# Kernel optimization log

Hardware: AMD Instinct MI355X
Metric: run time of the kernel (lower is better)

The kernel has to match this reference:

```python
import jax, jax.numpy as jnp
import numpy as np

HEADS = 16
HIDDEN = 1024
HEAD_DIM = HIDDEN // HEADS
NUM_RELATIONS = 100


def setup_inputs() -> dict:
    key = jax.random.key(0)
    ks = jax.random.split(key, 8)
    B, N, C = 4, 1024, HIDDEN
    x = jax.random.normal(ks[0], (B, N, C), dtype=jnp.float32)
    relations_mask = jax.random.randint(ks[1], (B, N, N), 0, NUM_RELATIONS, dtype=jnp.int64)
    s = 1.0 / np.sqrt(C)
    qkv_w = jax.random.uniform(ks[2], (3 * C, C), jnp.float32, -s, s)
    qkv_b = jax.random.uniform(ks[3], (3 * C,), jnp.float32, -s, s)
    proj_w = jax.random.uniform(ks[4], (C, C), jnp.float32, -s, s)
    proj_b = jax.random.uniform(ks[5], (C,), jnp.float32, -s, s)
    rel_emb = jax.random.normal(ks[6], (NUM_RELATIONS, HEAD_DIM), dtype=jnp.float32)
    return {"x": x, "relations_mask": relations_mask, "qkv_w": qkv_w,
            "qkv_b": qkv_b, "proj_w": proj_w, "proj_b": proj_b, "rel_emb": rel_emb}


def reference(x, relations_mask, qkv_w, qkv_b, proj_w, proj_b, rel_emb):
    B, N, C = x.shape
    H, d = HEADS, HEAD_DIM
    scale = d ** (-0.5)
    qkv = x @ qkv_w.T + qkv_b                       # [B, N, 3C]
    q, k, v = jnp.split(qkv, 3, axis=-1)
    to_heads = lambda t: t.reshape(B, N, H, d).transpose(0, 2, 1, 3)  # b h n d
    q, k, v = to_heads(q), to_heads(k), to_heads(v)
    dots = jnp.einsum('bhid,bhjd->bhij', q, k) * scale
    # einsum('bhij,bijd->bhijd', dots, bias).mean(-1) == dots * bias.mean(-1)
    rel_means = rel_emb.mean(-1)                    # [100]
    bias = rel_means[relations_mask]                # [B, N, N]
    dots = dots + dots * bias[:, None]              # broadcast over heads
    m = relations_mask.astype(dots.dtype)[:, None]  # hierarchy levels
    attn = jax.nn.softmax(dots * m + (1.0 - m) * (-1e9), axis=-1)
    out = jnp.einsum('bhij,bhjd->bhid', attn, v)
    out = out.transpose(0, 2, 1, 3).reshape(B, N, C)
    return out @ proj_w.T + proj_b
```

## Files before the change

### kernel.cpp

```cpp
#include <hip/hip_runtime.h>
#include <hip/hip_bf16.h>
#include <stdint.h>

constexpr int Bsz  = 4;
constexpr int Nseq = 1024;
constexpr int Cdim = 1024;
constexpr int Mrows = Bsz * Nseq;
constexpr int KD = 1024;
constexpr int BK = 64;
constexpr int NT = KD / BK;

typedef __attribute__((ext_vector_type(8))) short s16x8;
typedef __attribute__((ext_vector_type(4))) float f32x4;
typedef __attribute__((address_space(3))) unsigned char lds_b;
typedef __attribute__((address_space(1))) const unsigned char gbl_b;

__device__ inline short bf16_rne(float f) {
    union { float f; unsigned u; } c; c.f = f;
    unsigned u = c.u;
    u = u + 0x7FFFu + ((u >> 16) & 1u);
    return (short)(u >> 16);
}
__device__ inline float bf2f(unsigned short u) {
    union { unsigned u; float f; } c; c.u = ((unsigned)u) << 16;
    return c.f;
}

template <int N> __device__ __forceinline__ void waitv() {
    if constexpr (N == 0)      asm volatile("s_waitcnt vmcnt(0)" ::: "memory");
    else if constexpr (N == 4) asm volatile("s_waitcnt vmcnt(4)" ::: "memory");
    else if constexpr (N == 6) asm volatile("s_waitcnt vmcnt(6)" ::: "memory");
    else static_assert(N == 0, "unsupported vmcnt");
}

__global__ __launch_bounds__(256) void prep_kernel(const float* __restrict__ x,
                                                   const float* __restrict__ Wv,
                                                   const float* __restrict__ pw,
                                                   const float* __restrict__ bv,
                                                   const float* __restrict__ pb,
                                                   ushort* __restrict__ xb,
                                                   ushort* __restrict__ wvT,
                                                   ushort* __restrict__ pwb,
                                                   float* __restrict__ bias2) {
    const int bid = blockIdx.x;
    const int tid = threadIdx.x;
    if (bid < 256) {
        __shared__ ushort t[64][72];
        const int r0 = (bid >> 4) * 64, c0 = (bid & 15) * 64;
        const int lr = tid >> 4;
        const int lc = (tid & 15) * 4;
        #pragma unroll
        for (int p = 0; p < 4; ++p) {
            const int row = p * 16 + lr;
            const float4 v = *(const float4*)(Wv + (size_t)(r0 + row) * Cdim + c0 + lc);
            t[lc + 0][row] = (ushort)bf16_rne(v.x);
            t[lc + 1][row] = (ushort)bf16_rne(v.y);
            t[lc + 2][row] = (ushort)bf16_rne(v.z);
            t[lc + 3][row] = (ushort)bf16_rne(v.w);
        }
        __syncthreads();
        const int orow = tid >> 2;
        const int oc   = (tid & 3) * 16;
        const s16x8 a = *(const s16x8*)&t[orow][oc];
        const s16x8 b = *(const s16x8*)&t[orow][oc + 8];
        ushort* d = wvT + (size_t)(c0 + orow) * Cdim + r0 + oc;
        *(s16x8*)d = a;
        *(s16x8*)(d + 8) = b;
    } else if (bid < 512) {
        const int j = (bid - 256) * 4 + (tid >> 6);
        const int l = tid & 63;
        float s = 0.f;
        #pragma unroll
        for (int c = 0; c < 4; ++c) {
            const float4 w = *(const float4*)(pw + (size_t)j * Cdim + c * 256 + l * 4);
            const float4 b = *(const float4*)(bv + c * 256 + l * 4);
            s += w.x * b.x + w.y * b.y + w.z * b.z + w.w * b.w;
            ushort4 o;
            o.x = (ushort)bf16_rne(w.x); o.y = (ushort)bf16_rne(w.y);
            o.z = (ushort)bf16_rne(w.z); o.w = (ushort)bf16_rne(w.w);
            *(ushort4*)(pwb + (size_t)j * Cdim + c * 256 + l * 4) = o;
        }
        #pragma unroll
        for (int off = 32; off > 0; off >>= 1) s += __shfl_xor(s, off);
        if (l == 0) bias2[j] = s + pb[j];
    } else {
        constexpr int NX = Mrows * Cdim / 4;
        for (int i = (bid - 512) * 256 + tid; i < NX; i += 1536 * 256) {
            const float4 v = ((const float4*)x)[i];
            ushort4 o;
            o.x = (ushort)bf16_rne(v.x); o.y = (ushort)bf16_rne(v.y);
            o.z = (ushort)bf16_rne(v.z); o.w = (ushort)bf16_rne(v.w);
            ((ushort4*)xb)[i] = o;
        }
    }
}

template <int BM_, int BN_, bool OUT_BF16, bool HAS_BIAS>
__global__ __launch_bounds__(256) void gemm_bt(const ushort* __restrict__ A,
                                               const ushort* __restrict__ W,
                                               const float* __restrict__ bias,
                                               void* __restrict__ Cout,
                                               int Ncols) {
    constexpr int MI = BM_ / 32;
    constexpr int NI = BN_ / 32;
    constexpr int CA = BM_ / 32;
    constexpr int CB = BN_ / 32;
    __shared__ short As[3][BM_ * BK];
    __shared__ short Bs[3][BN_ * BK];
    const int tid  = threadIdx.x;
    const int lane = tid & 63;
    const int w    = tid >> 6;
    const int wr = w >> 1;
    const int wc = w & 1;
    const int fr = lane & 15;
    const int kg = lane >> 4;
    const int lr = lane >> 3;
    const int cs = lane & 7;

    const int arow0 = blockIdx.y * BM_;
    const int ncol0 = blockIdx.x * BN_;

    auto stage = [&](int b, int k0) {
        #pragma unroll
        for (int c = 0; c < CA; ++c) {
            const int r  = w * (BM_ / 4) + c * 8 + lr;
            const int gs = cs ^ (r & 7);
            __builtin_amdgcn_global_load_lds(
                (gbl_b*)(A + (size_t)(arow0 + r) * KD + k0 + gs * 8),
                (lds_b*)&As[b][(w * (BM_ / 4) + c * 8) * BK], 16, 0, 0);
        }
        #pragma unroll
        for (int c = 0; c < CB; ++c) {
            const int r  = w * (BN_ / 4) + c * 8 + lr;
            const int gs = cs ^ (r & 7);
            __builtin_amdgcn_global_load_lds(
                (gbl_b*)(W + (size_t)(ncol0 + r) * KD + k0 + gs * 8),
                (lds_b*)&Bs[b][(w * (BN_ / 4) + c * 8) * BK], 16, 0, 0);
        }
    };

    f32x4 acc[MI][NI] = {};

    stage(0, 0);
    stage(1, BK);

    int cur = 0;
    for (int t = 0; t < NT; ++t) {
        if (t < NT - 1) waitv<CA + CB>();
        else            waitv<0>();
        __builtin_amdgcn_s_barrier();
        __builtin_amdgcn_sched_barrier(0);

        if (t + 2 < NT) stage(cur + 2 >= 3 ? cur - 1 : cur + 2, (t + 2) * BK);

        s16x8 af[MI][2], bv_[NI][2];
        #pragma unroll
        for (int mi = 0; mi < MI; ++mi)
            #pragma unroll
            for (int ks = 0; ks < 2; ++ks) {
                const int row = wr * (BM_ / 2) + mi * 16 + fr;
                const int sl  = (ks * 4 + kg) ^ (row & 7);
                af[mi][ks] = *(const s16x8*)&As[cur][row * BK + sl * 8];
            }
        #pragma unroll
        for (int ni = 0; ni < NI; ++ni)
            #pragma unroll
            for (int ks = 0; ks < 2; ++ks) {
                const int row = wc * (BN_ / 2) + ni * 16 + fr;
                const int sl  = (ks * 4 + kg) ^ (row & 7);
                bv_[ni][ks] = *(const s16x8*)&Bs[cur][row * BK + sl * 8];
            }

        #pragma unroll
        for (int ks = 0; ks < 2; ++ks)
            #pragma unroll
            for (int mi = 0; mi < MI; ++mi)
                #pragma unroll
                for (int ni = 0; ni < NI; ++ni)
                    acc[mi][ni] = __builtin_amdgcn_mfma_f32_16x16x32_bf16(
                        af[mi][ks], bv_[ni][ks], acc[mi][ni], 0, 0, 0);

        cur = (cur + 1 == 3) ? 0 : cur + 1;
    }

    #pragma unroll
    for (int mi = 0; mi < MI; ++mi) {
        const int row0 = arow0 + wr * (BM_ / 2) + mi * 16 + kg * 4;
        #pragma unroll
        for (int ni = 0; ni < NI; ++ni) {
            const int col = ncol0 + wc * (BN_ / 2) + ni * 16 + fr;
            const float bs = HAS_BIAS ? bias[col] : 0.f;
            f32x4 r = acc[mi][ni];
            if (OUT_BF16) {
                ushort* o = (ushort*)Cout;
                #pragma unroll
                for (int j = 0; j < 4; ++j)
                    o[(size_t)(row0 + j) * Ncols + col] = (ushort)bf16_rne(r[j] + bs);
            } else {
                float* o = (float*)Cout;
                #pragma unroll
                for (int j = 0; j < 4; ++j)
                    o[(size_t)(row0 + j) * Ncols + col] = r[j] + bs;
            }
        }
    }
}

__global__ __launch_bounds__(256) void mask_avg_kernel(const int* __restrict__ mask,
                                                       const ushort* __restrict__ xb,
                                                       ushort* __restrict__ Z) {
    const int row = blockIdx.x;
    const int tid = threadIdx.x;
    const int lane = tid & 63;
    const int w = tid >> 6;
    const int b = row >> 10;
    const int* mrow = mask + (size_t)row * Nseq;

    __shared__ int wmax[4];
    __shared__ int wtot[4];
    __shared__ int idx[1024];

    const int4 mv = ((const int4*)mrow)[tid];
    int lm = max(max(mv.x, mv.y), max(mv.z, mv.w));
    #pragma unroll
    for (int off = 32; off > 0; off >>= 1) lm = max(lm, __shfl_xor(lm, off));
    if (lane == 0) wmax[w] = lm;
    __syncthreads();
    const int gmax = max(max(wmax[0], wmax[1]), max(wmax[2], wmax[3]));

    const int loc = (mv.x == gmax) + (mv.y == gmax) + (mv.z == gmax) + (mv.w == gmax);
    int s = loc;
    #pragma unroll
    for (int off = 1; off < 64; off <<= 1) {
        const int o = __shfl_up(s, off, 64);
        if (lane >= off) s += o;
    }
    if (lane == 63) wtot[w] = s;
    __syncthreads();
    int base = 0;
    #pragma unroll
    for (int w2 = 0; w2 < 4; ++w2) if (w2 < w) base += wtot[w2];
    const int n = wtot[0] + wtot[1] + wtot[2] + wtot[3];

    int pos = base + s - loc;
    if (mv.x == gmax) idx[pos++] = tid * 4 + 0;
    if (mv.y == gmax) idx[pos++] = tid * 4 + 1;
    if (mv.z == gmax) idx[pos++] = tid * 4 + 2;
    if (mv.w == gmax) idx[pos++] = tid * 4 + 3;
    __syncthreads();

    const ushort* xbb = xb + (size_t)(b << 10) * Cdim;
    float4 acc = make_float4(0.f, 0.f, 0.f, 0.f);
    for (int t = 0; t < n; ++t) {
        const ushort4 v = *(const ushort4*)(xbb + (size_t)idx[t] * Cdim + tid * 4);
        acc.x += bf2f(v.x); acc.y += bf2f(v.y);
        acc.z += bf2f(v.z); acc.w += bf2f(v.w);
    }
    const float inv = 1.0f / (float)n;
    ushort4 o;
    o.x = (ushort)bf16_rne(acc.x * inv); o.y = (ushort)bf16_rne(acc.y * inv);
    o.z = (ushort)bf16_rne(acc.z * inv); o.w = (ushort)bf16_rne(acc.w * inv);
    *(ushort4*)(Z + (size_t)row * Cdim + tid * 4) = o;
}

extern "C" void kernel_launch(void* const* d_in, const int* in_sizes, int n_in,
                              void* d_out, int out_size, void* d_ws, size_t ws_size,
                              hipStream_t stream) {
    const float* x      = (const float*)d_in[0];
    const int*   mask   = (const int*)d_in[1];
    const float* qkv_w  = (const float*)d_in[2];
    const float* qkv_b  = (const float*)d_in[3];
    const float* proj_w = (const float*)d_in[4];
    const float* proj_b = (const float*)d_in[5];
    float* out = (float*)d_out;

    ushort* xb    = (ushort*)d_ws;
    ushort* wvT   = xb   + (size_t)Mrows * Cdim;
    ushort* pwb   = wvT  + (size_t)Cdim * Cdim;
    ushort* W2b   = pwb  + (size_t)Cdim * Cdim;
    ushort* Zb    = W2b  + (size_t)Cdim * Cdim;
    float*  bias2 = (float*)(Zb + (size_t)Mrows * Cdim);

    const float* Wv = qkv_w + (size_t)2 * Cdim * Cdim;
    const float* bv = qkv_b + 2 * Cdim;

    prep_kernel<<<dim3(2048), 256, 0, stream>>>(x, Wv, proj_w, bv, proj_b,
                                                xb, wvT, pwb, bias2);
    mask_avg_kernel<<<dim3(Mrows), 256, 0, stream>>>(mask, xb, Zb);
    gemm_bt<64, 64, true, false><<<dim3(Cdim / 64, Cdim / 64), 256, 0, stream>>>(
        pwb, wvT, nullptr, W2b, Cdim);
    gemm_bt<64, 128, false, true><<<dim3(Cdim / 128, Mrows / 64), 256, 0, stream>>>(
        Zb, W2b, bias2, out, Cdim);
}
```

Baseline: 52.11 us.

## Fuse mask averaging into prep kernel, read fp32 x directly, retune GEMM pipeline

The x-to-bf16 conversion pass is removed. The masked-row averaging now reads fp32 x directly and runs inside the prep kernel, which drops one launch and one full read-write pass over x. The GEMM is reworked to use BK=32 with a 4-buffer, 3-stage-ahead prefetch and a new LDS swizzle. The final GEMM uses 128x128 tiles with a block-index swizzle for L2 locality. In exchange, the gather now moves twice as many bytes because it reads fp32 instead of bf16, and each K step does less MFMA work per barrier.

```diff
diff --git a/kernel.cpp b/kernel.cpp
--- a/kernel.cpp
+++ b/kernel.cpp
@@ -7,7 +7,7 @@
 constexpr int Cdim = 1024;
 constexpr int Mrows = Bsz * Nseq;
 constexpr int KD = 1024;
-constexpr int BK = 64;
+constexpr int BK = 32;
 constexpr int NT = KD / BK;
 
 typedef __attribute__((ext_vector_type(8))) short s16x8;
@@ -21,27 +21,21 @@
     u = u + 0x7FFFu + ((u >> 16) & 1u);
     return (short)(u >> 16);
 }
-__device__ inline float bf2f(unsigned short u) {
-    union { unsigned u; float f; } c; c.u = ((unsigned)u) << 16;
-    return c.f;
-}
 
 template <int N> __device__ __forceinline__ void waitv() {
     if constexpr (N == 0)      asm volatile("s_waitcnt vmcnt(0)" ::: "memory");
+    else if constexpr (N == 2) asm volatile("s_waitcnt vmcnt(2)" ::: "memory");
     else if constexpr (N == 4) asm volatile("s_waitcnt vmcnt(4)" ::: "memory");
-    else if constexpr (N == 6) asm volatile("s_waitcnt vmcnt(6)" ::: "memory");
+    else if constexpr (N == 8) asm volatile("s_waitcnt vmcnt(8)" ::: "memory");
     else static_assert(N == 0, "unsupported vmcnt");
 }
 
-__global__ __launch_bounds__(256) void prep_kernel(const float* __restrict__ x,
-                                                   const float* __restrict__ Wv,
-                                                   const float* __restrict__ pw,
-                                                   const float* __restrict__ bv,
-                                                   const float* __restrict__ pb,
-                                                   ushort* __restrict__ xb,
-                                                   ushort* __restrict__ wvT,
-                                                   ushort* __restrict__ pwb,
-                                                   float* __restrict__ bias2) {
+__global__ __launch_bounds__(256) void prep_mask_kernel(
+        const float* __restrict__ x, const int* __restrict__ mask,
+        const float* __restrict__ Wv, const float* __restrict__ pw,
+        const float* __restrict__ bv, const float* __restrict__ pb,
+        ushort* __restrict__ wvT, ushort* __restrict__ pwb,
+        float* __restrict__ bias2, ushort* __restrict__ Zb) {
     const int bid = blockIdx.x;
     const int tid = threadIdx.x;
     if (bid < 256) {
@@ -66,7 +60,9 @@
         ushort* d = wvT + (size_t)(c0 + orow) * Cdim + r0 + oc;
         *(s16x8*)d = a;
         *(s16x8*)(d + 8) = b;
-    } else if (bid < 512) {
+        return;
+    }
+    if (bid < 512) {
         const int j = (bid - 256) * 4 + (tid >> 6);
         const int l = tid & 63;
         float s = 0.f;
@@ -83,19 +79,71 @@
         #pragma unroll
         for (int off = 32; off > 0; off >>= 1) s += __shfl_xor(s, off);
         if (l == 0) bias2[j] = s + pb[j];
-    } else {
-        constexpr int NX = Mrows * Cdim / 4;
-        for (int i = (bid - 512) * 256 + tid; i < NX; i += 1536 * 256) {
-            const float4 v = ((const float4*)x)[i];
-            ushort4 o;
-            o.x = (ushort)bf16_rne(v.x); o.y = (ushort)bf16_rne(v.y);
-            o.z = (ushort)bf16_rne(v.z); o.w = (ushort)bf16_rne(v.w);
-            ((ushort4*)xb)[i] = o;
-        }
-    }
-}
-
-template <int BM_, int BN_, bool OUT_BF16, bool HAS_BIAS>
+        return;
+    }
+    __shared__ int wmax[4];
+    __shared__ int wtot[4];
+    __shared__ int idx[1024];
+    const int m   = bid - 512;
+    const int row = (m & 7) * 512 + (m >> 3);
+    const int lane = tid & 63;
+    const int w = tid >> 6;
+    const int b = row >> 10;
+    const int* mrow = mask + (size_t)row * Nseq;
+
+    const int4 mv = ((const int4*)mrow)[tid];
+    int lm = max(max(mv.x, mv.y), max(mv.z, mv.w));
+    #pragma unroll
+    for (int off = 32; off > 0; off >>= 1) lm = max(lm, __shfl_xor(lm, off));
+    if (lane == 0) wmax[w] = lm;
+    __syncthreads();
+    const int gmax = max(max(wmax[0], wmax[1]), max(wmax[2], wmax[3]));
+
+    const int loc = (mv.x == gmax) + (mv.y == gmax) + (mv.z == gmax) + (mv.w == gmax);
+    int s = loc;
+    #pragma unroll
+    for (int off = 1; off < 64; off <<= 1) {
+        const int o = __shfl_up(s, off, 64);
+        if (lane >= off) s += o;
+    }
+    if (lane == 63) wtot[w] = s;
+    __syncthreads();
+    int base = 0;
+    #pragma unroll
+    for (int w2 = 0; w2 < 4; ++w2) if (w2 < w) base += wtot[w2];
+    const int n = wtot[0] + wtot[1] + wtot[2] + wtot[3];
+
+    int pos = base + s - loc;
+    if (mv.x == gmax) idx[pos++] = tid * 4 + 0;
+    if (mv.y == gmax) idx[pos++] = tid * 4 + 1;
+    if (mv.z == gmax) idx[pos++] = tid * 4 + 2;
+    if (mv.w == gmax) idx[pos++] = tid * 4 + 3;
+    __syncthreads();
+
+    const float* xb_ = x + (size_t)(b << 10) * Cdim;
+    float4 a0 = make_float4(0.f, 0.f, 0.f, 0.f);
+    float4 a1 = make_float4(0.f, 0.f, 0.f, 0.f);
+    int t = 0;
+    for (; t + 1 < n; t += 2) {
+        const float4 v0 = *(const float4*)(xb_ + (size_t)idx[t] * Cdim + tid * 4);
+        const float4 v1 = *(const float4*)(xb_ + (size_t)idx[t + 1] * Cdim + tid * 4);
+        a0.x += v0.x; a0.y += v0.y; a0.z += v0.z; a0.w += v0.w;
+        a1.x += v1.x; a1.y += v1.y; a1.z += v1.z; a1.w += v1.w;
+    }
+    if (t < n) {
+        const float4 v = *(const float4*)(xb_ + (size_t)idx[t] * Cdim + tid * 4);
+        a0.x += v.x; a0.y += v.y; a0.z += v.z; a0.w += v.w;
+    }
+    const float inv = 1.0f / (float)n;
+    ushort4 o;
+    o.x = (ushort)bf16_rne((a0.x + a1.x) * inv);
+    o.y = (ushort)bf16_rne((a0.y + a1.y) * inv);
+    o.z = (ushort)bf16_rne((a0.z + a1.z) * inv);
+    o.w = (ushort)bf16_rne((a0.w + a1.w) * inv);
+    *(ushort4*)(Zb + (size_t)row * Cdim + tid * 4) = o;
+}
+
+template <int BM_, int BN_, bool OUT_BF16, bool HAS_BIAS, bool SWZ, int NTX>
 __global__ __launch_bounds__(256) void gemm_bt(const ushort* __restrict__ A,
                                                const ushort* __restrict__ W,
                                                const float* __restrict__ bias,
@@ -103,10 +151,12 @@
                                                int Ncols) {
     constexpr int MI = BM_ / 32;
     constexpr int NI = BN_ / 32;
-    constexpr int CA = BM_ / 32;
-    constexpr int CB = BN_ / 32;
-    __shared__ short As[3][BM_ * BK];
-    __shared__ short Bs[3][BN_ * BK];
+    constexpr int CA = BM_ / 64;
+    constexpr int CB = BN_ / 64;
+    constexpr int SI = CA + CB;
+    constexpr int RS = BK;
+    __shared__ short As[4][BM_ * BK];
+    __shared__ short Bs[4][BN_ * BK];
     const int tid  = threadIdx.x;
     const int lane = tid & 63;
     const int w    = tid >> 6;
@@ -114,73 +164,72 @@
     const int wc = w & 1;
     const int fr = lane & 15;
     const int kg = lane >> 4;
-    const int lr = lane >> 3;
-    const int cs = lane & 7;
-
-    const int arow0 = blockIdx.y * BM_;
-    const int ncol0 = blockIdx.x * BN_;
-
-    auto stage = [&](int b, int k0) {
+    const int srow  = lane >> 2;
+    const int sslot = lane & 3;
+
+    int bx, by;
+    if constexpr (SWZ) {
+        by = (blockIdx.x & 7) * 4 + ((blockIdx.x >> 3) & 3);
+        bx = blockIdx.x >> 5;
+    } else {
+        bx = blockIdx.x % NTX;
+        by = blockIdx.x / NTX;
+    }
+    const int arow0 = by * BM_;
+    const int ncol0 = bx * BN_;
+
+    auto stage = [&](int buf, int k0) {
         #pragma unroll
         for (int c = 0; c < CA; ++c) {
-            const int r  = w * (BM_ / 4) + c * 8 + lr;
-            const int gs = cs ^ (r & 7);
+            const int rbase = (w * CA + c) * 16;
+            const int r  = rbase + srow;
+            const int gs = sslot ^ (r & 3);
             __builtin_amdgcn_global_load_lds(
                 (gbl_b*)(A + (size_t)(arow0 + r) * KD + k0 + gs * 8),
-                (lds_b*)&As[b][(w * (BM_ / 4) + c * 8) * BK], 16, 0, 0);
+                (lds_b*)&As[buf][rbase * RS], 16, 0, 0);
         }
         #pragma unroll
         for (int c = 0; c < CB; ++c) {
-            const int r  = w * (BN_ / 4) + c * 8 + lr;
-            const int gs = cs ^ (r & 7);
+            const int rbase = (w * CB + c) * 16;
+            const int r  = rbase + srow;
+            const int gs = sslot ^ (r & 3);
             __builtin_amdgcn_global_load_lds(
                 (gbl_b*)(W + (size_t)(ncol0 + r) * KD + k0 + gs * 8),
-                (lds_b*)&Bs[b][(w * (BN_ / 4) + c * 8) * BK], 16, 0, 0);
+                (lds_b*)&Bs[buf][rbase * RS], 16, 0, 0);
         }
     };
 
     f32x4 acc[MI][NI] = {};
 
-    stage(0, 0);
-    stage(1, BK);
-
-    int cur = 0;
+    stage(0, 0); stage(1, BK); stage(2, 2 * BK);
+
     for (int t = 0; t < NT; ++t) {
-        if (t < NT - 1) waitv<CA + CB>();
-        else            waitv<0>();
+        if (t < NT - 2)      waitv<2 * SI>();
+        else if (t == NT - 2) waitv<SI>();
+        else                  waitv<0>();
         __builtin_amdgcn_s_barrier();
         __builtin_amdgcn_sched_barrier(0);
 
-        if (t + 2 < NT) stage(cur + 2 >= 3 ? cur - 1 : cur + 2, (t + 2) * BK);
-
-        s16x8 af[MI][2], bv_[NI][2];
+        if (t + 3 < NT) stage((t + 3) & 3, (t + 3) * BK);
+
+        const int cur = t & 3;
+        s16x8 af[MI], bf_[NI];
+        #pragma unroll
+        for (int mi = 0; mi < MI; ++mi) {
+            const int r = wr * (BM_ / 2) + mi * 16 + fr;
+            af[mi] = *(const s16x8*)&As[cur][r * RS + ((kg ^ (r & 3)) * 8)];
+        }
+        #pragma unroll
+        for (int ni = 0; ni < NI; ++ni) {
+            const int r = wc * (BN_ / 2) + ni * 16 + fr;
+            bf_[ni] = *(const s16x8*)&Bs[cur][r * RS + ((kg ^ (r & 3)) * 8)];
+        }
         #pragma unroll
         for (int mi = 0; mi < MI; ++mi)
             #pragma unroll
-            for (int ks = 0; ks < 2; ++ks) {
-                const int row = wr * (BM_ / 2) + mi * 16 + fr;
-                const int sl  = (ks * 4 + kg) ^ (row & 7);
-                af[mi][ks] = *(const s16x8*)&As[cur][row * BK + sl * 8];
-            }
-        #pragma unroll
-        for (int ni = 0; ni < NI; ++ni)
-            #pragma unroll
-            for (int ks = 0; ks < 2; ++ks) {
-                const int row = wc * (BN_ / 2) + ni * 16 + fr;
-                const int sl  = (ks * 4 + kg) ^ (row & 7);
-                bv_[ni][ks] = *(const s16x8*)&Bs[cur][row * BK + sl * 8];
-            }
-
-        #pragma unroll
-        for (int ks = 0; ks < 2; ++ks)
-            #pragma unroll
-            for (int mi = 0; mi < MI; ++mi)
-                #pragma unroll
-                for (int ni = 0; ni < NI; ++ni)
-                    acc[mi][ni] = __builtin_amdgcn_mfma_f32_16x16x32_bf16(
-                        af[mi][ks], bv_[ni][ks], acc[mi][ni], 0, 0, 0);
-
-        cur = (cur + 1 == 3) ? 0 : cur + 1;
+            for (int ni = 0; ni < NI; ++ni)
+                acc[mi][ni] = __builtin_amdgcn_mfma_f32_16x16x32_bf16(
+                    af[mi], bf_[ni], acc[mi][ni], 0, 0, 0);
     }
 
     #pragma unroll
@@ -206,63 +255,6 @@
     }
 }
 
-__global__ __launch_bounds__(256) void mask_avg_kernel(const int* __restrict__ mask,
-                                                       const ushort* __restrict__ xb,
-                                                       ushort* __restrict__ Z) {
-    const int row = blockIdx.x;
-    const int tid = threadIdx.x;
-    const int lane = tid & 63;
-    const int w = tid >> 6;
-    const int b = row >> 10;
-    const int* mrow = mask + (size_t)row * Nseq;
-
-    __shared__ int wmax[4];
-    __shared__ int wtot[4];
-    __shared__ int idx[1024];
-
-    const int4 mv = ((const int4*)mrow)[tid];
-    int lm = max(max(mv.x, mv.y), max(mv.z, mv.w));
-    #pragma unroll
-    for (int off = 32; off > 0; off >>= 1) lm = max(lm, __shfl_xor(lm, off));
-    if (lane == 0) wmax[w] = lm;
-    __syncthreads();
-    const int gmax = max(max(wmax[0], wmax[1]), max(wmax[2], wmax[3]));
-
-    const int loc = (mv.x == gmax) + (mv.y == gmax) + (mv.z == gmax) + (mv.w == gmax);
-    int s = loc;
-    #pragma unroll
-    for (int off = 1; off < 64; off <<= 1) {
-        const int o = __shfl_up(s, off, 64);
-        if (lane >= off) s += o;
-    }
-    if (lane == 63) wtot[w] = s;
-    __syncthreads();
-    int base = 0;
-    #pragma unroll
-    for (int w2 = 0; w2 < 4; ++w2) if (w2 < w) base += wtot[w2];
-    const int n = wtot[0] + wtot[1] + wtot[2] + wtot[3];
-
-    int pos = base + s - loc;
-    if (mv.x == gmax) idx[pos++] = tid * 4 + 0;
-    if (mv.y == gmax) idx[pos++] = tid * 4 + 1;
-    if (mv.z == gmax) idx[pos++] = tid * 4 + 2;
-    if (mv.w == gmax) idx[pos++] = tid * 4 + 3;
-    __syncthreads();
-
-    const ushort* xbb = xb + (size_t)(b << 10) * Cdim;
-    float4 acc = make_float4(0.f, 0.f, 0.f, 0.f);
-    for (int t = 0; t < n; ++t) {
-        const ushort4 v = *(const ushort4*)(xbb + (size_t)idx[t] * Cdim + tid * 4);
-        acc.x += bf2f(v.x); acc.y += bf2f(v.y);
-        acc.z += bf2f(v.z); acc.w += bf2f(v.w);
-    }
-    const float inv = 1.0f / (float)n;
-    ushort4 o;
-    o.x = (ushort)bf16_rne(acc.x * inv); o.y = (ushort)bf16_rne(acc.y * inv);
-    o.z = (ushort)bf16_rne(acc.z * inv); o.w = (ushort)bf16_rne(acc.w * inv);
-    *(ushort4*)(Z + (size_t)row * Cdim + tid * 4) = o;
-}
-
 extern "C" void kernel_launch(void* const* d_in, const int* in_sizes, int n_in,
                               void* d_out, int out_size, void* d_ws, size_t ws_size,
                               hipStream_t stream) {
@@ -274,8 +266,7 @@
     const float* proj_b = (const float*)d_in[5];
     float* out = (float*)d_out;
 
-    ushort* xb    = (ushort*)d_ws;
-    ushort* wvT   = xb   + (size_t)Mrows * Cdim;
+    ushort* wvT   = (ushort*)d_ws;
     ushort* pwb   = wvT  + (size_t)Cdim * Cdim;
     ushort* W2b   = pwb  + (size_t)Cdim * Cdim;
     ushort* Zb    = W2b  + (size_t)Cdim * Cdim;
@@ -284,11 +275,10 @@
     const float* Wv = qkv_w + (size_t)2 * Cdim * Cdim;
     const float* bv = qkv_b + 2 * Cdim;
 
-    prep_kernel<<<dim3(2048), 256, 0, stream>>>(x, Wv, proj_w, bv, proj_b,
-                                                xb, wvT, pwb, bias2);
-    mask_avg_kernel<<<dim3(Mrows), 256, 0, stream>>>(mask, xb, Zb);
-    gemm_bt<64, 64, true, false><<<dim3(Cdim / 64, Cdim / 64), 256, 0, stream>>>(
+    prep_mask_kernel<<<dim3(512 + Mrows), 256, 0, stream>>>(
+        x, mask, Wv, proj_w, bv, proj_b, wvT, pwb, bias2, Zb);
+    gemm_bt<64, 64, true, false, false, 16><<<dim3(256), 256, 0, stream>>>(
         pwb, wvT, nullptr, W2b, Cdim);
-    gemm_bt<64, 128, false, true><<<dim3(Cdim / 128, Mrows / 64), 256, 0, stream>>>(
+    gemm_bt<128, 128, false, true, true, 8><<<dim3(256), 256, 0, stream>>>(
         Zb, W2b, bias2, out, Cdim);
 }
```

New measurement: 57.85 us. +11.0%, slower.
